# Kernel tuning notes

Hardware: AMD Instinct MI355X
Metric: run time of the kernel (lower is better)

## Reference

```python
import jax, jax.numpy as jnp
import numpy as np

INPUT_DIM = 1024
HIDDEN_DIM = 1024


def setup_inputs() -> dict:
    key = jax.random.key(0)
    k1, k2, k3, k4, k5 = jax.random.split(key, 5)
    B, T = 64, 512
    bound_h = 1.0 / np.sqrt(HIDDEN_DIM)
    bound_x = 1.0 / np.sqrt(INPUT_DIM)
    return {
        "x_seq": jax.random.normal(k1, (B, T, INPUT_DIM), dtype=jnp.float32),
        "W_h": jax.random.uniform(k2, (HIDDEN_DIM, HIDDEN_DIM), jnp.float32, -bound_h, bound_h),
        "b_h": jax.random.uniform(k3, (HIDDEN_DIM,), jnp.float32, -bound_h, bound_h),
        "W_x": jax.random.uniform(k4, (HIDDEN_DIM, INPUT_DIM), jnp.float32, -bound_x, bound_x),
        "b_x": jax.random.uniform(k5, (HIDDEN_DIM,), jnp.float32, -bound_x, bound_x),
    }


def reference(x_seq, W_h, b_h, W_x, b_x):
    # Precompute input projection for all timesteps as one batched GEMM:
    # xp: [B, T, H]
    xp = jnp.einsum("bti,hi->bth", x_seq, W_x) + b_x
    B = x_seq.shape[0]
    h0 = jnp.zeros((B, HIDDEN_DIM), dtype=x_seq.dtype)

    def step(h, xp_t):
        # h: [B, H], xp_t: [B, H]
        h_new = jnp.tanh(h @ W_h.T + b_h + xp_t)
        return h_new, None

    # scan over time: xp transposed to [T, B, H]
    h_final, _ = jax.lax.scan(step, h0, jnp.swapaxes(xp, 0, 1))
    return h_final  # [B, H] — last hidden state per batch element
```

## Files before the change

### kernel.cpp

```cpp
#include <hip/hip_runtime.h>
#include <cmath>


#define Bsz 64
#define Tsz 512
#define Hsz 1024

typedef float  f32x4 __attribute__((ext_vector_type(4)));
typedef short  s16x8 __attribute__((ext_vector_type(8)));

__device__ __forceinline__ unsigned short f2bf(float f) {
  unsigned u = __float_as_uint(f);
  u += 0x7fff + ((u >> 16) & 1);
  return (unsigned short)(u >> 16);
}

__device__ __forceinline__ void pack8(unsigned short* d, float4 v0, float4 v1) {
  d[0] = f2bf(v0.x); d[1] = f2bf(v0.y); d[2] = f2bf(v0.z); d[3] = f2bf(v0.w);
  d[4] = f2bf(v1.x); d[5] = f2bf(v1.y); d[6] = f2bf(v1.z); d[7] = f2bf(v1.w);
}

__device__ __forceinline__ float fast_tanh(float x) {
  float e = __expf(2.0f * x);
  return 1.0f - 2.0f / (e + 1.0f);
}

__global__ __launch_bounds__(256) void xp_gemm_kernel(
    const float* __restrict__ x, const float* __restrict__ Wx,
    const float* __restrict__ bx, const float* __restrict__ bh,
    float* __restrict__ xp) {
  __shared__ unsigned short Al[64 * 32];
  __shared__ unsigned short Bl[64 * 32];

  const int tid  = threadIdx.x;
  const int w    = tid >> 6;
  const int lane = tid & 63;
  const int m    = lane & 15;
  const int q    = lane >> 4;
  const int row0 = blockIdx.x * 64;
  const int col0 = blockIdx.y * 64;

  f32x4 acc[4];
#pragma unroll
  for (int i = 0; i < 4; ++i) acc[i] = (f32x4){0.f, 0.f, 0.f, 0.f};

  const int sr = tid >> 2;
  const int sc = tid & 3;
  const int sw = sc ^ ((sr >> 1) & 3);

  for (int kt = 0; kt < 32; ++kt) {
    const int k0 = kt * 32 + sc * 8;
    {
      const float* p = x + (size_t)(row0 + sr) * 1024 + k0;
      pack8(&Al[sr * 32 + sw * 8], *(const float4*)p, *(const float4*)(p + 4));
    }
    {
      const float* p = Wx + (size_t)(col0 + sr) * 1024 + k0;
      pack8(&Bl[sr * 32 + sw * 8], *(const float4*)p, *(const float4*)(p + 4));
    }
    __syncthreads();
    const int arow = w * 16 + m;
    s16x8 a = *(const s16x8*)&Al[arow * 32 + ((q ^ ((arow >> 1) & 3)) << 3)];
#pragma unroll
    for (int nt = 0; nt < 4; ++nt) {
      const int nrow = nt * 16 + m;
      s16x8 b = *(const s16x8*)&Bl[nrow * 32 + ((q ^ ((nrow >> 1) & 3)) << 3)];
      acc[nt] = __builtin_amdgcn_mfma_f32_16x16x32_bf16(a, b, acc[nt], 0, 0, 0);
    }
    __syncthreads();
  }

#pragma unroll
  for (int nt = 0; nt < 4; ++nt) {
    const int col  = col0 + nt * 16 + m;
    const float bias = bx[col] + bh[col];
#pragma unroll
    for (int r = 0; r < 4; ++r) {
      const int rowg = row0 + w * 16 + q * 4 + r;
      const int b = rowg >> 9;
      const int t = rowg & 511;
      xp[(size_t)t * (Bsz * Hsz) + b * Hsz + col] = acc[nt][r] + bias;
    }
  }
}

__global__ __launch_bounds__(128) void rnn_scan_kernel(
    const float* __restrict__ Wh, const float* __restrict__ xp,
    float* __restrict__ out,
    unsigned short* __restrict__ h0buf, unsigned short* __restrict__ h1buf,
    unsigned* __restrict__ flags) {
  __shared__ unsigned short Wl[32 * 1024];
  __shared__ unsigned short Tr[2][16 * 20];

  const int tid  = threadIdx.x;
  const int w    = tid >> 6;
  const int lane = tid & 63;
  const int m    = lane & 15;
  const int q    = lane >> 4;
  const int gb   = blockIdx.x >> 5;
  const int gj   = blockIdx.x & 31;
  const int rb   = gb * 16;
  const int j0   = gj * 32;

  for (int jr = 0; jr < 32; ++jr) {
    const float* p = Wh + (size_t)(j0 + jr) * 1024 + tid * 8;
    unsigned short* d = &Wl[jr * 1024 + ((((unsigned)tid) ^ (jr & 7)) << 3)];
    pack8(d, *(const float4*)p, *(const float4*)(p + 4));
  }
  __syncthreads();

  const int colg = j0 + w * 16 + m;
  const int jl   = w * 16 + m;

  unsigned* grpflags = flags + gb * 32 * 16;
  unsigned* myflag   = grpflags + gj * 16;
  const unsigned* pollflag = grpflags + (lane & 31) * 16;

  const int t_br = (lane >> 1) & 15;
  const int t_c0 = (lane >> 5) * 8 + (lane & 1) * 4;

  for (int t = 0; t < Tsz; ++t) {
    const unsigned short* hc = (t & 1) ? h1buf : h0buf;
    unsigned short*       hn = (t & 1) ? h0buf : h1buf;

    float xv[4];
#pragma unroll
    for (int r = 0; r < 4; ++r)
      xv[r] = xp[(size_t)t * (Bsz * Hsz) + (rb + q * 4 + r) * Hsz + colg];

    f32x4 acc0 = (f32x4){0.f, 0.f, 0.f, 0.f};
    f32x4 acc1 = (f32x4){0.f, 0.f, 0.f, 0.f};

    if (t > 0) {
      const unsigned long long* src =
          (const unsigned long long*)(hc + gb * 16384);
      const int loff = (q * 16 + m) * 2;

      unsigned v = __hip_atomic_load(pollflag, __ATOMIC_RELAXED,
                                     __HIP_MEMORY_SCOPE_AGENT);
      int wm = (int)__builtin_ctzll(~__ballot(v >= (unsigned)t) |
                                    0xFFFFFFFF00000000ull);
#pragma unroll
      for (int g = 0; g < 4; ++g) {
        while (wm < (g + 1) * 8) {
          __builtin_amdgcn_s_sleep(1);
          unsigned v2 = __hip_atomic_load(pollflag, __ATOMIC_RELAXED,
                                          __HIP_MEMORY_SCOPE_AGENT);
          wm = (int)__builtin_ctzll(~__ballot(v2 >= (unsigned)t) |
                                    0xFFFFFFFF00000000ull);
        }
        union { unsigned long long u[2]; s16x8 v; } a[8];
#pragma unroll
        for (int j = 0; j < 8; ++j) {
          const unsigned long long* cp = src + (g * 8 + j) * 128 + loff;
          a[j].u[0] = __hip_atomic_load(cp,     __ATOMIC_RELAXED, __HIP_MEMORY_SCOPE_AGENT);
          a[j].u[1] = __hip_atomic_load(cp + 1, __ATOMIC_RELAXED, __HIP_MEMORY_SCOPE_AGENT);
        }
#pragma unroll
        for (int j = 0; j < 8; ++j) {
          const int c = (g * 8 + j) * 4 + q;
          s16x8 b = *(const s16x8*)&Wl[jl * 1024 + ((c ^ (jl & 7)) << 3)];
          if (j & 1)
            acc1 = __builtin_amdgcn_mfma_f32_16x16x32_bf16(a[j].v, b, acc1, 0, 0, 0);
          else
            acc0 = __builtin_amdgcn_mfma_f32_16x16x32_bf16(a[j].v, b, acc0, 0, 0, 0);
        }
      }
    }
    f32x4 acc = acc0 + acc1;

    float hv[4];
#pragma unroll
    for (int r = 0; r < 4; ++r) hv[r] = fast_tanh(acc[r] + xv[r]);

    if (t == Tsz - 1) {
#pragma unroll
      for (int r = 0; r < 4; ++r)
        out[(rb + q * 4 + r) * Hsz + colg] = hv[r];
    } else {
      unsigned short* S = &Tr[w][0];
#pragma unroll
      for (int r = 0; r < 4; ++r)
        S[(q * 4 + r) * 20 + m] = f2bf(hv[r]);
      __asm__ __volatile__("" ::: "memory");
      unsigned long long tv =
          *(const volatile unsigned long long*)&S[t_br * 20 + t_c0];
      __asm__ __volatile__("" ::: "memory");
      unsigned long long* dst =
          (unsigned long long*)(hn + gb * 16384 + gj * 512 + w * 256) + lane;
      __hip_atomic_store(dst, tv, __ATOMIC_RELAXED, __HIP_MEMORY_SCOPE_AGENT);

      __syncthreads();
      if (tid == 0)
        __hip_atomic_store(myflag, (unsigned)(t + 1), __ATOMIC_RELAXED,
                           __HIP_MEMORY_SCOPE_AGENT);
    }
  }
}

extern "C" void kernel_launch(void* const* d_in, const int* in_sizes, int n_in,
                              void* d_out, int out_size, void* d_ws, size_t ws_size,
                              hipStream_t stream) {
  (void)in_sizes; (void)n_in; (void)out_size; (void)ws_size;
  const float* x  = (const float*)d_in[0];
  const float* Wh = (const float*)d_in[1];
  const float* bh = (const float*)d_in[2];
  const float* Wx = (const float*)d_in[3];
  const float* bx = (const float*)d_in[4];
  float* out = (float*)d_out;

  char* ws = (char*)d_ws;
  unsigned*       flags = (unsigned*)ws;
  unsigned short* h0    = (unsigned short*)(ws + 65536);
  unsigned short* h1    = (unsigned short*)(ws + 65536 + 131072);
  float*          xp    = (float*)(ws + (1 << 20));

  hipMemsetAsync(d_ws, 0, 16384, stream);

  dim3 g1(Bsz * Tsz / 64, Hsz / 64);
  xp_gemm_kernel<<<g1, dim3(256), 0, stream>>>(x, Wx, bx, bh, xp);
  rnn_scan_kernel<<<dim3(128), dim3(128), 0, stream>>>(Wh, xp, out, h0, h1, flags);
}
```

Before: 1.836 ms.

## Replace flag-based step sync with tagged 4-deep ring buffer for hidden state

Removes the per-block flag plus barrier handshake. Each hidden-state bf16 value is now packed with its timestep tag in a 32-bit word and stored to a 4-slot ring, so consumers can validate the data they load directly instead of polling flags. The grid changes to 256 single-wave blocks, each owning 16 hidden columns, and the MFMA operands are swapped so outputs come out transposed for float4 xp loads and stores. Loads of the next group are double-buffered against compute. The cost is twice the traffic per h value, and correctness now depends on the tag matching on every word.

```diff
diff --git a/kernel.cpp b/kernel.cpp
--- a/kernel.cpp
+++ b/kernel.cpp
@@ -84,116 +84,133 @@
   }
 }
 
-__global__ __launch_bounds__(128) void rnn_scan_kernel(
+
+#define LOADG(D, g)                                                           \
+  do {                                                                        \
+    _Pragma("unroll")                                                         \
+    for (int f_ = 0; f_ < 8; ++f_) {                                          \
+      const unsigned long long* fb_ = rbase + ((g) * 8 + f_) * 256;           \
+      D[f_ * 4 + 0] = __hip_atomic_load(fb_,      __ATOMIC_RELAXED, __HIP_MEMORY_SCOPE_AGENT); \
+      D[f_ * 4 + 1] = __hip_atomic_load(fb_ + 1,  __ATOMIC_RELAXED, __HIP_MEMORY_SCOPE_AGENT); \
+      D[f_ * 4 + 2] = __hip_atomic_load(fb_ + 32, __ATOMIC_RELAXED, __HIP_MEMORY_SCOPE_AGENT); \
+      D[f_ * 4 + 3] = __hip_atomic_load(fb_ + 33, __ATOMIC_RELAXED, __HIP_MEMORY_SCOPE_AGENT); \
+    }                                                                         \
+  } while (0)
+
+#define CHECK4(D, f)                                                          \
+  (int)((((unsigned)D[(f) * 4 + 0] & 0xFFFFu) == tg) &                        \
+        (((unsigned)D[(f) * 4 + 1] & 0xFFFFu) == tg) &                        \
+        (((unsigned)D[(f) * 4 + 2] & 0xFFFFu) == tg) &                        \
+        (((unsigned)D[(f) * 4 + 3] & 0xFFFFu) == tg))
+
+#define FIXG(D, g)                                                            \
+  do {                                                                        \
+    _Pragma("unroll")                                                         \
+    for (int f_ = 0; f_ < 8; ++f_) {                                          \
+      int ok_ = CHECK4(D, f_);                                                \
+      while (!__all(ok_)) {                                                   \
+        const unsigned long long* fb_ = rbase + ((g) * 8 + f_) * 256;         \
+        D[f_ * 4 + 0] = __hip_atomic_load(fb_,      __ATOMIC_RELAXED, __HIP_MEMORY_SCOPE_AGENT); \
+        D[f_ * 4 + 1] = __hip_atomic_load(fb_ + 1,  __ATOMIC_RELAXED, __HIP_MEMORY_SCOPE_AGENT); \
+        D[f_ * 4 + 2] = __hip_atomic_load(fb_ + 32, __ATOMIC_RELAXED, __HIP_MEMORY_SCOPE_AGENT); \
+        D[f_ * 4 + 3] = __hip_atomic_load(fb_ + 33, __ATOMIC_RELAXED, __HIP_MEMORY_SCOPE_AGENT); \
+        ok_ = CHECK4(D, f_);                                                  \
+      }                                                                       \
+    }                                                                         \
+  } while (0)
+
+#define COMPUTEG(D, g)                                                        \
+  do {                                                                        \
+    _Pragma("unroll")                                                         \
+    for (int f_ = 0; f_ < 8; ++f_) {                                          \
+      const int kk_ = (g) * 8 + f_;                                           \
+      union { unsigned u[4]; s16x8 v; } hb_;                                  \
+      hb_.u[0] = __builtin_amdgcn_perm((unsigned)(D[f_ * 4 + 0] >> 32),       \
+                                       (unsigned)D[f_ * 4 + 0], 0x07060302u); \
+      hb_.u[1] = __builtin_amdgcn_perm((unsigned)(D[f_ * 4 + 1] >> 32),       \
+                                       (unsigned)D[f_ * 4 + 1], 0x07060302u); \
+      hb_.u[2] = __builtin_amdgcn_perm((unsigned)(D[f_ * 4 + 2] >> 32),       \
+                                       (unsigned)D[f_ * 4 + 2], 0x07060302u); \
+      hb_.u[3] = __builtin_amdgcn_perm((unsigned)(D[f_ * 4 + 3] >> 32),       \
+                                       (unsigned)D[f_ * 4 + 3], 0x07060302u); \
+      s16x8 wf_ = *(const s16x8*)&Wl[m * 1024 + (((kk_ * 4 + q) ^ (m & 7)) << 3)]; \
+      f32x4& ac_ = ((kk_ & 3) == 0) ? acc0 : ((kk_ & 3) == 1) ? acc1          \
+                  : ((kk_ & 3) == 2) ? acc2 : acc3;                           \
+      ac_ = __builtin_amdgcn_mfma_f32_16x16x32_bf16(wf_, hb_.v, ac_, 0, 0, 0);\
+    }                                                                         \
+  } while (0)
+
+__global__ __launch_bounds__(64) void rnn_scan_kernel(
     const float* __restrict__ Wh, const float* __restrict__ xp,
-    float* __restrict__ out,
-    unsigned short* __restrict__ h0buf, unsigned short* __restrict__ h1buf,
-    unsigned* __restrict__ flags) {
-  __shared__ unsigned short Wl[32 * 1024];
-  __shared__ unsigned short Tr[2][16 * 20];
-
-  const int tid  = threadIdx.x;
-  const int w    = tid >> 6;
-  const int lane = tid & 63;
+    float* __restrict__ out, unsigned long long* __restrict__ ring) {
+  __shared__ unsigned short Wl[16 * 1024];
+
+  const int lane = threadIdx.x & 63;
   const int m    = lane & 15;
   const int q    = lane >> 4;
-  const int gb   = blockIdx.x >> 5;
-  const int gj   = blockIdx.x & 31;
+  const int gb   = blockIdx.x >> 6;
+  const int gj   = blockIdx.x & 63;
+  const int j0   = gj * 16;
   const int rb   = gb * 16;
-  const int j0   = gj * 32;
-
-  for (int jr = 0; jr < 32; ++jr) {
-    const float* p = Wh + (size_t)(j0 + jr) * 1024 + tid * 8;
-    unsigned short* d = &Wl[jr * 1024 + ((((unsigned)tid) ^ (jr & 7)) << 3)];
-    pack8(d, *(const float4*)p, *(const float4*)(p + 4));
+
+  for (int i = 0; i < 32; ++i) {
+    const int jr = i >> 1;
+    const int c  = (i & 1) * 64 + lane;
+    const float* p = Wh + (size_t)(j0 + jr) * 1024 + c * 8;
+    pack8(&Wl[jr * 1024 + ((c ^ (jr & 7)) << 3)],
+          *(const float4*)p, *(const float4*)(p + 4));
   }
   __syncthreads();
 
-  const int colg = j0 + w * 16 + m;
-  const int jl   = w * 16 + m;
-
-  unsigned* grpflags = flags + gb * 32 * 16;
-  unsigned* myflag   = grpflags + gj * 16;
-  const unsigned* pollflag = grpflags + (lane & 31) * 16;
-
-  const int t_br = (lane >> 1) & 15;
-  const int t_c0 = (lane >> 5) * 8 + (lane & 1) * 4;
+  const size_t grpoff = (size_t)gb * 8192;
+  const int    ldoff  = q * 64 + m * 2;
+  const int    stoff  = (gj * 4 + q) * 32 + m * 2;
 
   for (int t = 0; t < Tsz; ++t) {
-    const unsigned short* hc = (t & 1) ? h1buf : h0buf;
-    unsigned short*       hn = (t & 1) ? h0buf : h1buf;
-
-    float xv[4];
-#pragma unroll
-    for (int r = 0; r < 4; ++r)
-      xv[r] = xp[(size_t)t * (Bsz * Hsz) + (rb + q * 4 + r) * Hsz + colg];
+    const float4 xv = *(const float4*)(
+        xp + (size_t)t * (Bsz * Hsz) + (size_t)(rb + m) * Hsz + j0 + q * 4);
 
     f32x4 acc0 = (f32x4){0.f, 0.f, 0.f, 0.f};
     f32x4 acc1 = (f32x4){0.f, 0.f, 0.f, 0.f};
+    f32x4 acc2 = (f32x4){0.f, 0.f, 0.f, 0.f};
+    f32x4 acc3 = (f32x4){0.f, 0.f, 0.f, 0.f};
 
     if (t > 0) {
-      const unsigned long long* src =
-          (const unsigned long long*)(hc + gb * 16384);
-      const int loff = (q * 16 + m) * 2;
-
-      unsigned v = __hip_atomic_load(pollflag, __ATOMIC_RELAXED,
-                                     __HIP_MEMORY_SCOPE_AGENT);
-      int wm = (int)__builtin_ctzll(~__ballot(v >= (unsigned)t) |
-                                    0xFFFFFFFF00000000ull);
-#pragma unroll
-      for (int g = 0; g < 4; ++g) {
-        while (wm < (g + 1) * 8) {
-          __builtin_amdgcn_s_sleep(1);
-          unsigned v2 = __hip_atomic_load(pollflag, __ATOMIC_RELAXED,
-                                          __HIP_MEMORY_SCOPE_AGENT);
-          wm = (int)__builtin_ctzll(~__ballot(v2 >= (unsigned)t) |
-                                    0xFFFFFFFF00000000ull);
-        }
-        union { unsigned long long u[2]; s16x8 v; } a[8];
-#pragma unroll
-        for (int j = 0; j < 8; ++j) {
-          const unsigned long long* cp = src + (g * 8 + j) * 128 + loff;
-          a[j].u[0] = __hip_atomic_load(cp,     __ATOMIC_RELAXED, __HIP_MEMORY_SCOPE_AGENT);
-          a[j].u[1] = __hip_atomic_load(cp + 1, __ATOMIC_RELAXED, __HIP_MEMORY_SCOPE_AGENT);
-        }
-#pragma unroll
-        for (int j = 0; j < 8; ++j) {
-          const int c = (g * 8 + j) * 4 + q;
-          s16x8 b = *(const s16x8*)&Wl[jl * 1024 + ((c ^ (jl & 7)) << 3)];
-          if (j & 1)
-            acc1 = __builtin_amdgcn_mfma_f32_16x16x32_bf16(a[j].v, b, acc1, 0, 0, 0);
-          else
-            acc0 = __builtin_amdgcn_mfma_f32_16x16x32_bf16(a[j].v, b, acc0, 0, 0, 0);
-        }
-      }
-    }
-    f32x4 acc = acc0 + acc1;
-
+      const unsigned tg = (unsigned)t;
+      const unsigned long long* rbase =
+          ring + (size_t)(t & 3) * 32768 + grpoff + ldoff;
+
+      unsigned long long A[32], B[32];
+      LOADG(A, 0);
+      LOADG(B, 1);
+      FIXG(A, 0); COMPUTEG(A, 0);
+      LOADG(A, 2);
+      FIXG(B, 1); COMPUTEG(B, 1);
+      LOADG(B, 3);
+      FIXG(A, 2); COMPUTEG(A, 2);
+      FIXG(B, 3); COMPUTEG(B, 3);
+    }
+
+    const f32x4 accs = (acc0 + acc1) + (acc2 + acc3);
     float hv[4];
 #pragma unroll
-    for (int r = 0; r < 4; ++r) hv[r] = fast_tanh(acc[r] + xv[r]);
+    for (int r = 0; r < 4; ++r) hv[r] = fast_tanh(accs[r] + xv.x * 0.f + ((const float*)&xv)[r]);
 
     if (t == Tsz - 1) {
-#pragma unroll
-      for (int r = 0; r < 4; ++r)
-        out[(rb + q * 4 + r) * Hsz + colg] = hv[r];
+      *(float4*)&out[(size_t)(rb + m) * Hsz + j0 + q * 4] =
+          make_float4(hv[0], hv[1], hv[2], hv[3]);
     } else {
-      unsigned short* S = &Tr[w][0];
-#pragma unroll
-      for (int r = 0; r < 4; ++r)
-        S[(q * 4 + r) * 20 + m] = f2bf(hv[r]);
-      __asm__ __volatile__("" ::: "memory");
-      unsigned long long tv =
-          *(const volatile unsigned long long*)&S[t_br * 20 + t_c0];
-      __asm__ __volatile__("" ::: "memory");
-      unsigned long long* dst =
-          (unsigned long long*)(hn + gb * 16384 + gj * 512 + w * 256) + lane;
-      __hip_atomic_store(dst, tv, __ATOMIC_RELAXED, __HIP_MEMORY_SCOPE_AGENT);
-
-      __syncthreads();
-      if (tid == 0)
-        __hip_atomic_store(myflag, (unsigned)(t + 1), __ATOMIC_RELAXED,
-                           __HIP_MEMORY_SCOPE_AGENT);
+      const unsigned tg1 = (unsigned)(t + 1);
+      const unsigned long long s0 =
+          (unsigned long long)(tg1 | ((unsigned)f2bf(hv[0]) << 16)) |
+          ((unsigned long long)(tg1 | ((unsigned)f2bf(hv[1]) << 16)) << 32);
+      const unsigned long long s1 =
+          (unsigned long long)(tg1 | ((unsigned)f2bf(hv[2]) << 16)) |
+          ((unsigned long long)(tg1 | ((unsigned)f2bf(hv[3]) << 16)) << 32);
+      unsigned long long* wb =
+          ring + (size_t)((t + 1) & 3) * 32768 + grpoff + stoff;
+      __hip_atomic_store(wb,     s0, __ATOMIC_RELAXED, __HIP_MEMORY_SCOPE_AGENT);
+      __hip_atomic_store(wb + 1, s1, __ATOMIC_RELAXED, __HIP_MEMORY_SCOPE_AGENT);
     }
   }
 }
@@ -210,14 +227,12 @@
   float* out = (float*)d_out;
 
   char* ws = (char*)d_ws;
-  unsigned*       flags = (unsigned*)ws;
-  unsigned short* h0    = (unsigned short*)(ws + 65536);
-  unsigned short* h1    = (unsigned short*)(ws + 65536 + 131072);
-  float*          xp    = (float*)(ws + (1 << 20));
-
-  hipMemsetAsync(d_ws, 0, 16384, stream);
+  unsigned long long* ring = (unsigned long long*)ws;
+  float*              xp   = (float*)(ws + (1 << 20));
+
+  hipMemsetAsync(d_ws, 0, 1 << 20, stream);
 
   dim3 g1(Bsz * Tsz / 64, Hsz / 64);
   xp_gemm_kernel<<<g1, dim3(256), 0, stream>>>(x, Wx, bx, bh, xp);
-  rnn_scan_kernel<<<dim3(128), dim3(128), 0, stream>>>(Wh, xp, out, h0, h1, flags);
-}
+  rnn_scan_kernel<<<dim3(256), dim3(64), 0, stream>>>(Wh, xp, out, ring);
+}
```

Result: slower. 5.357 ms (+191.7%).
